# Optimization experiments

Hardware: AMD Instinct MI355X
Metric: run time of the kernel (lower is better)

## Reference

```python
import jax, jax.numpy as jnp
import numpy as np

N_NODES = 100000
N_EDGES = 1600000
IN_CH, HID_CH, OUT_CH = 8, 64, 2


def setup_inputs() -> dict:
    key = jax.random.key(0)
    ks = jax.random.split(key, 8)
    x = jax.random.normal(ks[0], (N_NODES, IN_CH), dtype=jnp.float32)
    edge_index = jax.random.randint(ks[1], (2, N_EDGES), 0, N_NODES, dtype=jnp.int64)
    s1 = 1.0 / np.sqrt(IN_CH)
    s2 = 1.0 / np.sqrt(HID_CH)
    W_l1 = jax.random.normal(ks[2], (HID_CH, IN_CH), dtype=jnp.float32) * s1
    b_l1 = jax.random.normal(ks[3], (HID_CH,), dtype=jnp.float32) * s1
    W_r1 = jax.random.normal(ks[4], (HID_CH, IN_CH), dtype=jnp.float32) * s1
    W_l2 = jax.random.normal(ks[5], (OUT_CH, HID_CH), dtype=jnp.float32) * s2
    b_l2 = jax.random.normal(ks[6], (OUT_CH,), dtype=jnp.float32) * s2
    W_r2 = jax.random.normal(ks[7], (OUT_CH, HID_CH), dtype=jnp.float32) * s2
    return {"x": x, "edge_index": edge_index, "W_l1": W_l1, "b_l1": b_l1,
            "W_r1": W_r1, "W_l2": W_l2, "b_l2": b_l2, "W_r2": W_r2}


def _sage_conv(x, edge_index, W_l, b_l, W_r):
    # PyG SAGEConv (aggr='mean', root_weight=True):
    #   out = lin_l(mean_{j in N(i)} x_j) + lin_r(x_i)
    src, dst = edge_index[0], edge_index[1]
    n = x.shape[0]
    msgs = x[src]                                             # [E, F] gather
    summed = jax.ops.segment_sum(msgs, dst, num_segments=n)   # [N, F] scatter-add
    cnt = jax.ops.segment_sum(jnp.ones((src.shape[0],), x.dtype), dst,
                              num_segments=n)                 # [N]
    aggr = summed / jnp.maximum(cnt, 1.0)[:, None]            # scatter-mean
    return aggr @ W_l.T + b_l + x @ W_r.T


def reference(x, edge_index, W_l1, b_l1, W_r1, W_l2, b_l2, W_r2):
    h = _sage_conv(x, edge_index, W_l1, b_l1, W_r1)
    h = jax.nn.relu(h)
    # Dropout(0.3) is identity in eval mode (deterministic baseline).
    out = _sage_conv(h, edge_index, W_l2, b_l2, W_r2)
    return out
```

## Files before the change

kernel.cpp:

```cpp
#include <hip/hip_runtime.h>

#define N_NODES 100000
#define N_EDGES 1600000
#define IN_CH 8
#define HID_CH 64
#define OUT_CH 2

#define R2   1024
#define RN   98
#define CAP  1920
#define CSTRIDE 16

#define NCHUNK 32
#define CH_E (N_EDGES / NCHUNK)
#define NW   16
#define WSTG 552

#define WS_BUCKET (R2 * CSTRIDE)
#define WS_OFFDEG (WS_BUCKET + R2 * CAP)
#define WS_G      (WS_OFFDEG + R2 * RN)

__global__ __launch_bounds__(1024) void bucket_own(
        const int* __restrict__ src, const int* __restrict__ dst,
        int* __restrict__ cursor, int* __restrict__ bucket) {
    __shared__ int stg[NW * WSTG];
    __shared__ int wcnt[NW];
    __shared__ int cnt[R2];
    __shared__ int cur[R2];
    int tid = threadIdx.x;
    int w = tid >> 6;
    unsigned own = blockIdx.x >> 5;
    int chunk = blockIdx.x & 31;
    if (tid < R2) cnt[tid] = 0;
    if (tid < NW) wcnt[tid] = 0;
    __syncthreads();

    const int2* d2 = (const int2*)(dst + (size_t)chunk * CH_E);
    const int2* s2 = (const int2*)(src + (size_t)chunk * CH_E);
    int* mystg = stg + w * WSTG;
    for (int i = tid; i < CH_E / 2; i += 1024) {
        int2 d = d2[i];
        int2 s = s2[i];
        {
            unsigned r = (unsigned)d.x / RN;
            if ((r & 7) == own) {
                unsigned dl = (unsigned)d.x - r * RN;
                int p = atomicAdd(&wcnt[w], 1);
                if (p < WSTG) {
                    mystg[p] = (int)(((r >> 3) << 24) | (dl << 17) | (unsigned)s.x);
                    atomicAdd(&cnt[r], 1);
                }
            }
        }
        {
            unsigned r = (unsigned)d.y / RN;
            if ((r & 7) == own) {
                unsigned dl = (unsigned)d.y - r * RN;
                int p = atomicAdd(&wcnt[w], 1);
                if (p < WSTG) {
                    mystg[p] = (int)(((r >> 3) << 24) | (dl << 17) | (unsigned)s.y);
                    atomicAdd(&cnt[r], 1);
                }
            }
        }
    }
    __syncthreads();

    for (int i = tid; i < R2; i += 1024) {
        if (((unsigned)i & 7) == own) {
            int c = cnt[i];
            cur[i] = (c > 0) ? atomicAdd(&cursor[i * CSTRIDE], c) : 0;
        }
    }
    __syncthreads();

    int mycnt = wcnt[w];
    if (mycnt > WSTG) mycnt = WSTG;
    for (int j = tid & 63; j < mycnt; j += 64) {
        int e = mystg[j];
        unsigned r = (((unsigned)e >> 24) << 3) | own;
        int slot = atomicAdd(&cur[r], 1);
        if (slot < CAP)
            bucket[(size_t)r * CAP + slot] = e & 0x00FFFFFF;
    }
}

__global__ __launch_bounds__(512) void sage1_range(
        const int* __restrict__ bucket, const int* __restrict__ cursor,
        const float* __restrict__ x,
        const float* __restrict__ W_l1, const float* __restrict__ b_l1,
        const float* __restrict__ W_r1,
        const float* __restrict__ W_l2, const float* __restrict__ b_l2,
        const float* __restrict__ W_r2,
        int* __restrict__ csr, int* __restrict__ offdeg,
        float* __restrict__ g, float* __restrict__ out_rt) {
    __shared__ int raw[CAP];
    __shared__ int seg[CAP];
    __shared__ int scnt[128];
    __shared__ int soff[128];
    __shared__ int scur[128];
    __shared__ int wtot[2];
    __shared__ float sWl[HID_CH * IN_CH];
    __shared__ float sWr[HID_CH * IN_CH];
    __shared__ float sb[HID_CH];
    __shared__ float sWl2[OUT_CH * HID_CH];
    __shared__ float sWr2[OUT_CH * HID_CH];
    __shared__ float sb2[OUT_CH];

    int tid = threadIdx.x;
    for (int i = tid; i < HID_CH * IN_CH; i += 512) {
        sWl[i] = W_l1[i];
        sWr[i] = W_r1[i];
    }
    for (int i = tid; i < HID_CH; i += 512) sb[i] = b_l1[i];
    for (int i = tid; i < OUT_CH * HID_CH; i += 512) {
        sWl2[i] = W_l2[i];
        sWr2[i] = W_r2[i];
    }
    if (tid < OUT_CH) sb2[tid] = b_l2[tid];
    if (tid < 128) scnt[tid] = 0;

    int r = blockIdx.x;
    int len = cursor[r * CSTRIDE];
    if (len > CAP) len = CAP;
    const int* bin = bucket + (size_t)r * CAP;
    for (int j = tid; j < len; j += 512) raw[j] = bin[j];
    __syncthreads();

    for (int j = tid; j < len; j += 512) atomicAdd(&scnt[raw[j] >> 17], 1);
    __syncthreads();

    int lane = tid & 63;
    if (tid < 128) {
        int v = scnt[tid];
        int incl = v;
        #pragma unroll
        for (int d = 1; d < 64; d <<= 1) {
            int t2 = __shfl_up(incl, d);
            if (lane >= d) incl += t2;
        }
        if (lane == 63) wtot[tid >> 6] = incl;
        soff[tid] = incl - v;
    }
    __syncthreads();
    if (tid < 128) {
        int o = soff[tid] + ((tid >= 64) ? wtot[0] : 0);
        soff[tid] = o;
        scur[tid] = o;
    }
    __syncthreads();

    for (int j = tid; j < len; j += 512) {
        int w = raw[j];
        int p = atomicAdd(&scur[w >> 17], 1);
        seg[p] = w & 0x1FFFF;
    }
    __syncthreads();

    int* cw = csr + (size_t)r * CAP;
    for (int j = tid; j < len; j += 512) cw[j] = seg[j];

    int q = tid >> 2;
    int l = tid & 3;
    int node = r * RN + q;
    if (q < RN && node < N_NODES) {
        int o = soff[q];
        int dn = scnt[q];
        if (l == 0) offdeg[node] = o | (dn << 16);

        float acc[IN_CH];
        #pragma unroll
        for (int c = 0; c < IN_CH; c++) acc[c] = 0.0f;
        for (int j = o + l; j < o + dn; j += 4) {
            int s = seg[j];
            const float4* xs = (const float4*)(x + (size_t)s * IN_CH);
            float4 a = xs[0];
            float4 b = xs[1];
            acc[0] += a.x; acc[1] += a.y; acc[2] += a.z; acc[3] += a.w;
            acc[4] += b.x; acc[5] += b.y; acc[6] += b.z; acc[7] += b.w;
        }
        #pragma unroll
        for (int c = 0; c < IN_CH; c++) {
            acc[c] += __shfl_xor(acc[c], 1);
            acc[c] += __shfl_xor(acc[c], 2);
        }
        float inv = 1.0f / fmaxf((float)dn, 1.0f);
        float ag[IN_CH], xa[IN_CH];
        #pragma unroll
        for (int c = 0; c < IN_CH; c++) ag[c] = acc[c] * inv;
        const float4* xp = (const float4*)(x + (size_t)node * IN_CH);
        float4 x0 = xp[0], x1 = xp[1];
        xa[0] = x0.x; xa[1] = x0.y; xa[2] = x0.z; xa[3] = x0.w;
        xa[4] = x1.x; xa[5] = x1.y; xa[6] = x1.z; xa[7] = x1.w;

        float g0 = 0.f, g1 = 0.f, r0 = 0.f, r1 = 0.f;
        int k0 = l * 16;
        #pragma unroll 4
        for (int kk = k0; kk < k0 + 16; kk++) {
            float hk = sb[kk];
            #pragma unroll
            for (int c = 0; c < IN_CH; c++) {
                hk += sWl[kk * IN_CH + c] * ag[c];
                hk += sWr[kk * IN_CH + c] * xa[c];
            }
            hk = fmaxf(hk, 0.0f);
            g0 += sWl2[kk] * hk;
            g1 += sWl2[HID_CH + kk] * hk;
            r0 += sWr2[kk] * hk;
            r1 += sWr2[HID_CH + kk] * hk;
        }
        g0 += __shfl_xor(g0, 1); g0 += __shfl_xor(g0, 2);
        g1 += __shfl_xor(g1, 1); g1 += __shfl_xor(g1, 2);
        r0 += __shfl_xor(r0, 1); r0 += __shfl_xor(r0, 2);
        r1 += __shfl_xor(r1, 1); r1 += __shfl_xor(r1, 2);
        if (l == 0) {
            g[(size_t)node * 2 + 0] = g0;
            g[(size_t)node * 2 + 1] = g1;
            float2 rt;
            rt.x = r0 + sb2[0];
            rt.y = r1 + sb2[1];
            *(float2*)(out_rt + (size_t)node * 2) = rt;
        }
    }
}

__global__ __launch_bounds__(256) void sage2_kernel(
        const int* __restrict__ csr, const int* __restrict__ offdeg,
        const float* __restrict__ g, float* __restrict__ out) {
    int t = blockIdx.x * blockDim.x + threadIdx.x;
    int node = t >> 2;
    int l = t & 3;
    if (node >= N_NODES) return;
    int r = node / RN;
    int od = offdeg[node];
    int o = od & 0xFFFF;
    int dn = od >> 16;
    const int* seg = csr + (size_t)r * CAP;
    float a0 = 0.f, a1 = 0.f;
    for (int j = o + l; j < o + dn; j += 4) {
        int s = seg[j];
        float2 gv = *(const float2*)(g + (size_t)s * 2);
        a0 += gv.x;
        a1 += gv.y;
    }
    a0 += __shfl_xor(a0, 1); a0 += __shfl_xor(a0, 2);
    a1 += __shfl_xor(a1, 1); a1 += __shfl_xor(a1, 2);
    if (l == 0) {
        float inv = 1.0f / fmaxf((float)dn, 1.0f);
        float2 rt = *(const float2*)(out + (size_t)node * 2);
        float2 ov;
        ov.x = a0 * inv + rt.x;
        ov.y = a1 * inv + rt.y;
        *(float2*)(out + (size_t)node * 2) = ov;
    }
}

extern "C" void kernel_launch(void* const* d_in, const int* in_sizes, int n_in,
                              void* d_out, int out_size, void* d_ws, size_t ws_size,
                              hipStream_t stream) {
    const float* x    = (const float*)d_in[0];
    const int*   ei   = (const int*)d_in[1];
    const float* W_l1 = (const float*)d_in[2];
    const float* b_l1 = (const float*)d_in[3];
    const float* W_r1 = (const float*)d_in[4];
    const float* W_l2 = (const float*)d_in[5];
    const float* b_l2 = (const float*)d_in[6];
    const float* W_r2 = (const float*)d_in[7];
    float* out = (float*)d_out;

    const int* src = ei;
    const int* dst = ei + N_EDGES;

    int*   cursor = (int*)d_ws;
    int*   bucket = (int*)d_ws + WS_BUCKET;
    int*   offdeg = (int*)d_ws + WS_OFFDEG;
    float* g      = (float*)d_ws + WS_G;

    hipMemsetAsync(cursor, 0, R2 * CSTRIDE * sizeof(int), stream);

    bucket_own<<<NCHUNK * 8, 1024, 0, stream>>>(src, dst, cursor, bucket);
    sage1_range<<<R2, 512, 0, stream>>>(bucket, cursor, x,
                                        W_l1, b_l1, W_r1, W_l2, b_l2, W_r2,
                                        bucket , offdeg, g, out);
    sage2_kernel<<<(4 * N_NODES + 255) / 256, 256, 0, stream>>>(bucket, offdeg, g, out);
}
```

Baseline: 134.3 us.

## Replace global atomic cursors with fixed per-chunk bucket spans and length headers

Each bucketing block now writes its edges for a range into a private fixed-size span (per range, per chunk) with a length header, instead of reserving space through global atomic cursors. This removes the memset launch, the per-range counting pass and the global atomics. The consumer kernel now reads all 4096 slots per range, including empty ones, and filters by the header lengths. It adds extra read traffic, a larger workspace and a per-span cap of 127 edges, and a separate CSR buffer.

Measured after the change: 140.6 us. 4.7% more time.

```diff
diff --git a/kernel.cpp b/kernel.cpp
--- a/kernel.cpp
+++ b/kernel.cpp
@@ -9,29 +9,29 @@
 #define R2   1024
 #define RN   98
 #define CAP  1920
-#define CSTRIDE 16
 
 #define NCHUNK 32
 #define CH_E (N_EDGES / NCHUNK)
 #define NW   16
 #define WSTG 552
-
-#define WS_BUCKET (R2 * CSTRIDE)
-#define WS_OFFDEG (WS_BUCKET + R2 * CAP)
+#define SPANCAP 128
+#define SLOTS (NCHUNK * SPANCAP)
+
+#define WS_CSR    (R2 * SLOTS)
+#define WS_OFFDEG (WS_CSR + R2 * CAP)
 #define WS_G      (WS_OFFDEG + R2 * RN)
 
 __global__ __launch_bounds__(1024) void bucket_own(
         const int* __restrict__ src, const int* __restrict__ dst,
-        int* __restrict__ cursor, int* __restrict__ bucket) {
+        int* __restrict__ bucket) {
     __shared__ int stg[NW * WSTG];
     __shared__ int wcnt[NW];
-    __shared__ int cnt[R2];
     __shared__ int cur[R2];
     int tid = threadIdx.x;
     int w = tid >> 6;
     unsigned own = blockIdx.x >> 5;
     int chunk = blockIdx.x & 31;
-    if (tid < R2) cnt[tid] = 0;
+    if (tid < R2) cur[tid] = 0;
     if (tid < NW) wcnt[tid] = 0;
     __syncthreads();
 
@@ -46,10 +46,8 @@
             if ((r & 7) == own) {
                 unsigned dl = (unsigned)d.x - r * RN;
                 int p = atomicAdd(&wcnt[w], 1);
-                if (p < WSTG) {
+                if (p < WSTG)
                     mystg[p] = (int)(((r >> 3) << 24) | (dl << 17) | (unsigned)s.x);
-                    atomicAdd(&cnt[r], 1);
-                }
             }
         }
         {
@@ -57,19 +55,9 @@
             if ((r & 7) == own) {
                 unsigned dl = (unsigned)d.y - r * RN;
                 int p = atomicAdd(&wcnt[w], 1);
-                if (p < WSTG) {
+                if (p < WSTG)
                     mystg[p] = (int)(((r >> 3) << 24) | (dl << 17) | (unsigned)s.y);
-                    atomicAdd(&cnt[r], 1);
-                }
             }
-        }
-    }
-    __syncthreads();
-
-    for (int i = tid; i < R2; i += 1024) {
-        if (((unsigned)i & 7) == own) {
-            int c = cnt[i];
-            cur[i] = (c > 0) ? atomicAdd(&cursor[i * CSTRIDE], c) : 0;
         }
     }
     __syncthreads();
@@ -80,13 +68,22 @@
         int e = mystg[j];
         unsigned r = (((unsigned)e >> 24) << 3) | own;
         int slot = atomicAdd(&cur[r], 1);
-        if (slot < CAP)
-            bucket[(size_t)r * CAP + slot] = e & 0x00FFFFFF;
+        if (slot < SPANCAP - 1)
+            bucket[(size_t)(r * NCHUNK + chunk) * SPANCAP + 1 + slot] = e & 0x00FFFFFF;
+    }
+    __syncthreads();
+
+    for (int i = tid; i < R2; i += 1024) {
+        if (((unsigned)i & 7) == own) {
+            int c = cur[i];
+            if (c > SPANCAP - 1) c = SPANCAP - 1;
+            bucket[(size_t)(i * NCHUNK + chunk) * SPANCAP] = c;
+        }
     }
 }
 
 __global__ __launch_bounds__(512) void sage1_range(
-        const int* __restrict__ bucket, const int* __restrict__ cursor,
+        const int* __restrict__ bucket,
         const float* __restrict__ x,
         const float* __restrict__ W_l1, const float* __restrict__ b_l1,
         const float* __restrict__ W_r1,
@@ -94,7 +91,7 @@
         const float* __restrict__ W_r2,
         int* __restrict__ csr, int* __restrict__ offdeg,
         float* __restrict__ g, float* __restrict__ out_rt) {
-    __shared__ int raw[CAP];
+    __shared__ int raw[SLOTS];
     __shared__ int seg[CAP];
     __shared__ int scnt[128];
     __shared__ int soff[128];
@@ -121,13 +118,15 @@
     if (tid < 128) scnt[tid] = 0;
 
     int r = blockIdx.x;
-    int len = cursor[r * CSTRIDE];
-    if (len > CAP) len = CAP;
-    const int* bin = bucket + (size_t)r * CAP;
-    for (int j = tid; j < len; j += 512) raw[j] = bin[j];
-    __syncthreads();
-
-    for (int j = tid; j < len; j += 512) atomicAdd(&scnt[raw[j] >> 17], 1);
+    const int* bin = bucket + (size_t)r * SLOTS;
+    for (int j = tid; j < SLOTS; j += 512) raw[j] = bin[j];
+    __syncthreads();
+
+    for (int j = tid; j < SLOTS; j += 512) {
+        int sl = j & (SPANCAP - 1);
+        int len = raw[j & ~(SPANCAP - 1)];
+        if (sl >= 1 && sl <= len) atomicAdd(&scnt[raw[j] >> 17], 1);
+    }
     __syncthreads();
 
     int lane = tid & 63;
@@ -150,15 +149,21 @@
     }
     __syncthreads();
 
-    for (int j = tid; j < len; j += 512) {
-        int w = raw[j];
-        int p = atomicAdd(&scur[w >> 17], 1);
-        seg[p] = w & 0x1FFFF;
-    }
-    __syncthreads();
-
+    for (int j = tid; j < SLOTS; j += 512) {
+        int sl = j & (SPANCAP - 1);
+        int len = raw[j & ~(SPANCAP - 1)];
+        if (sl >= 1 && sl <= len) {
+            int w = raw[j];
+            int p = atomicAdd(&scur[w >> 17], 1);
+            seg[p] = w & 0x1FFFF;
+        }
+    }
+    __syncthreads();
+
+    int total = wtot[0] + wtot[1];
+    if (total > CAP) total = CAP;
     int* cw = csr + (size_t)r * CAP;
-    for (int j = tid; j < len; j += 512) cw[j] = seg[j];
+    for (int j = tid; j < total; j += 512) cw[j] = seg[j];
 
     int q = tid >> 2;
     int l = tid & 3;
@@ -271,16 +276,14 @@
     const int* src = ei;
     const int* dst = ei + N_EDGES;
 
-    int*   cursor = (int*)d_ws;
-    int*   bucket = (int*)d_ws + WS_BUCKET;
+    int*   bucket = (int*)d_ws;
+    int*   csr    = (int*)d_ws + WS_CSR;
     int*   offdeg = (int*)d_ws + WS_OFFDEG;
     float* g      = (float*)d_ws + WS_G;
 
-    hipMemsetAsync(cursor, 0, R2 * CSTRIDE * sizeof(int), stream);
-
-    bucket_own<<<NCHUNK * 8, 1024, 0, stream>>>(src, dst, cursor, bucket);
-    sage1_range<<<R2, 512, 0, stream>>>(bucket, cursor, x,
+    bucket_own<<<NCHUNK * 8, 1024, 0, stream>>>(src, dst, bucket);
+    sage1_range<<<R2, 512, 0, stream>>>(bucket, x,
                                         W_l1, b_l1, W_r1, W_l2, b_l2, W_r2,
-                                        bucket , offdeg, g, out);
-    sage2_kernel<<<(4 * N_NODES + 255) / 256, 256, 0, stream>>>(bucket, offdeg, g, out);
-}
+                                        csr, offdeg, g, out);
+    sage2_kernel<<<(4 * N_NODES + 255) / 256, 256, 0, stream>>>(csr, offdeg, g, out);
+}
```

## Replace owner-filtered bucketing with per-chunk local counting sort

Applied to the files above, without the earlier changes.

The bucketing kernel now gives each block a contiguous edge chunk and counting-sorts it in shared memory. It counts per destination range, runs a block-wide scan, reserves global slots with one atomic per range, then writes contiguous runs out to the bucket array. This replaces the old scheme in which each edge chunk was read by eight owner blocks, each keeping only its one-eighth of ranges. That cuts redundant global reads and scattered writes, at the cost of a second pass over dst and a smaller grid of 128 blocks using a large shared-memory stage.

Result: slower. 138.5 us (+3.1%).

```diff
diff --git a/kernel.cpp b/kernel.cpp
--- a/kernel.cpp
+++ b/kernel.cpp
@@ -11,77 +11,96 @@
 #define CAP  1920
 #define CSTRIDE 16
 
-#define NCHUNK 32
-#define CH_E (N_EDGES / NCHUNK)
-#define NW   16
-#define WSTG 552
+#define NB   128
+#define CH   (N_EDGES / NB)
+#define CH2  (CH / 2)
 
 #define WS_BUCKET (R2 * CSTRIDE)
 #define WS_OFFDEG (WS_BUCKET + R2 * CAP)
 #define WS_G      (WS_OFFDEG + R2 * RN)
 
-__global__ __launch_bounds__(1024) void bucket_own(
+__global__ __launch_bounds__(1024) void bucket_sort(
         const int* __restrict__ src, const int* __restrict__ dst,
         int* __restrict__ cursor, int* __restrict__ bucket) {
-    __shared__ int stg[NW * WSTG];
-    __shared__ int wcnt[NW];
+    __shared__ int stage[CH];
     __shared__ int cnt[R2];
-    __shared__ int cur[R2];
+    __shared__ int loc[R2];
+    __shared__ int lcur[R2];
+    __shared__ int base[R2];
+    __shared__ int wsum[16];
     int tid = threadIdx.x;
     int w = tid >> 6;
-    unsigned own = blockIdx.x >> 5;
-    int chunk = blockIdx.x & 31;
-    if (tid < R2) cnt[tid] = 0;
-    if (tid < NW) wcnt[tid] = 0;
-    __syncthreads();
-
-    const int2* d2 = (const int2*)(dst + (size_t)chunk * CH_E);
-    const int2* s2 = (const int2*)(src + (size_t)chunk * CH_E);
-    int* mystg = stg + w * WSTG;
-    for (int i = tid; i < CH_E / 2; i += 1024) {
-        int2 d = d2[i];
-        int2 s = s2[i];
+    int lane = tid & 63;
+
+    cnt[tid] = 0;
+    __syncthreads();
+
+    const int2* dch = (const int2*)(dst + (size_t)blockIdx.x * CH);
+    const int2* sch = (const int2*)(src + (size_t)blockIdx.x * CH);
+
+    for (int i = tid; i < CH2; i += 1024) {
+        int2 d = dch[i];
+        atomicAdd(&cnt[(unsigned)d.x / RN], 1);
+        atomicAdd(&cnt[(unsigned)d.y / RN], 1);
+    }
+    __syncthreads();
+
+    int v = cnt[tid];
+    int incl = v;
+    #pragma unroll
+    for (int dd = 1; dd < 64; dd <<= 1) {
+        int t2 = __shfl_up(incl, dd);
+        if (lane >= dd) incl += t2;
+    }
+    if (lane == 63) wsum[w] = incl;
+    loc[tid] = incl - v;
+    __syncthreads();
+    if (w == 0 && lane < 16) {
+        int s = wsum[lane];
+        int si = s;
+        #pragma unroll
+        for (int dd = 1; dd < 16; dd <<= 1) {
+            int t2 = __shfl_up(si, dd);
+            if (lane >= dd) si += t2;
+        }
+        wsum[lane] = si - s;
+    }
+    __syncthreads();
+    {
+        int o = loc[tid] + wsum[w];
+        loc[tid] = o;
+        lcur[tid] = o;
+        base[tid] = (v > 0) ? atomicAdd(&cursor[tid * CSTRIDE], v) : 0;
+    }
+    __syncthreads();
+
+    for (int i = tid; i < CH2; i += 1024) {
+        int2 d = dch[i];
+        int2 s = sch[i];
         {
             unsigned r = (unsigned)d.x / RN;
-            if ((r & 7) == own) {
-                unsigned dl = (unsigned)d.x - r * RN;
-                int p = atomicAdd(&wcnt[w], 1);
-                if (p < WSTG) {
-                    mystg[p] = (int)(((r >> 3) << 24) | (dl << 17) | (unsigned)s.x);
-                    atomicAdd(&cnt[r], 1);
-                }
-            }
+            unsigned dl = (unsigned)d.x - r * RN;
+            int p = atomicAdd(&lcur[r], 1);
+            stage[p] = (int)((dl << 17) | (unsigned)s.x);
         }
         {
             unsigned r = (unsigned)d.y / RN;
-            if ((r & 7) == own) {
-                unsigned dl = (unsigned)d.y - r * RN;
-                int p = atomicAdd(&wcnt[w], 1);
-                if (p < WSTG) {
-                    mystg[p] = (int)(((r >> 3) << 24) | (dl << 17) | (unsigned)s.y);
-                    atomicAdd(&cnt[r], 1);
-                }
-            }
-        }
-    }
-    __syncthreads();
-
-    for (int i = tid; i < R2; i += 1024) {
-        if (((unsigned)i & 7) == own) {
-            int c = cnt[i];
-            cur[i] = (c > 0) ? atomicAdd(&cursor[i * CSTRIDE], c) : 0;
-        }
-    }
-    __syncthreads();
-
-    int mycnt = wcnt[w];
-    if (mycnt > WSTG) mycnt = WSTG;
-    for (int j = tid & 63; j < mycnt; j += 64) {
-        int e = mystg[j];
-        unsigned r = (((unsigned)e >> 24) << 3) | own;
-        int slot = atomicAdd(&cur[r], 1);
-        if (slot < CAP)
-            bucket[(size_t)r * CAP + slot] = e & 0x00FFFFFF;
+            unsigned dl = (unsigned)d.y - r * RN;
+            int p = atomicAdd(&lcur[r], 1);
+            stage[p] = (int)((dl << 17) | (unsigned)s.y);
+        }
+    }
+    __syncthreads();
+
+    for (int r = (w << 6); r < (w << 6) + 64; ++r) {
+        int c = cnt[r];
+        int b = base[r];
+        int lo = loc[r];
+        for (int j = lane; j < c; j += 64) {
+            int slot = b + j;
+            if (slot < CAP)
+                bucket[(size_t)r * CAP + slot] = stage[lo + j];
+        }
     }
 }
 
@@ -278,7 +297,7 @@
 
     hipMemsetAsync(cursor, 0, R2 * CSTRIDE * sizeof(int), stream);
 
-    bucket_own<<<NCHUNK * 8, 1024, 0, stream>>>(src, dst, cursor, bucket);
+    bucket_sort<<<NB, 1024, 0, stream>>>(src, dst, cursor, bucket);
     sage1_range<<<R2, 512, 0, stream>>>(bucket, cursor, x,
                                         W_l1, b_l1, W_r1, W_l2, b_l2, W_r2,
                                         bucket , offdeg, g, out);
```
